# Kernel optimization log

Measured on AMD Instinct MI355X. Metric: run time of the kernel, lower is better.

The kernel has to match this reference:

```python
import jax, jax.numpy as jnp
import numpy as np

B, T, D_IN, UNITS, D_OUT = 64, 2048, 64, 128, 1
ODE_UNFOLDS = 6  # fused semi-implicit Euler sub-steps per timestep


def setup_inputs() -> dict:
    key = jax.random.key(0)
    ks = jax.random.split(key, 8)
    s = lambda fan: 1.0 / np.sqrt(fan).astype(np.float32)
    return {
        "x": jax.random.normal(ks[0], (B, T, D_IN), jnp.float32),
        "kernel": jax.random.normal(ks[1], (D_IN, UNITS), jnp.float32) * s(D_IN),
        "recurrent_kernel": jax.random.normal(ks[2], (UNITS, UNITS), jnp.float32) * s(UNITS),
        "bias": jnp.zeros((UNITS,), jnp.float32),
        "tau": jax.random.uniform(ks[3], (UNITS,), jnp.float32, 0.5, 2.0),  # positive time constants
        "A": jax.random.normal(ks[4], (UNITS,), jnp.float32),  # reversal potentials
        "out_kernel": jax.random.normal(ks[5], (UNITS, D_OUT), jnp.float32) * s(UNITS),
        "out_bias": jnp.zeros((D_OUT,), jnp.float32),
    }


def _ltc_scan(x_proj, recurrent_kernel, tau, A):
    # x_proj: [B, T, U] precomputed input projection (+bias)
    dt = jnp.float32(1.0 / ODE_UNFOLDS)
    inv_tau = 1.0 / tau  # [U]

    def step(h, xp):  # h: [B,U], xp: [B,U]
        # LTC fused ODE solver: semi-implicit Euler, ODE_UNFOLDS sub-steps
        for _ in range(ODE_UNFOLDS):
            f = jax.nn.sigmoid(xp + h @ recurrent_kernel)  # gating nonlinearity
            h = (h + dt * f * A) / (1.0 + dt * (inv_tau + f))
        return h, h

    h0 = jnp.zeros((x_proj.shape[0], tau.shape[0]), x_proj.dtype)
    _, hs = jax.lax.scan(step, h0, jnp.swapaxes(x_proj, 0, 1))  # scan over time
    return jnp.swapaxes(hs, 0, 1)  # [B, T, U]


def reference(x, kernel, recurrent_kernel, bias, tau, A, out_kernel, out_bias):
    # input projection hoisted out of the recurrence (invariant across unfolds)
    x_proj = jnp.einsum("bti,iu->btu", x, kernel) + bias  # [B,T,U]
    hs = _ltc_scan(x_proj, recurrent_kernel, tau, A)       # return_sequences=True
    return hs @ out_kernel + out_bias                       # Dense(output_dim) -> [B,T,1]
```

## Files before the change

kernel.cpp:

```cpp
#include <hip/hip_runtime.h>

#define TSTEPS  2048
#define DIN     64
#define UNITS   128
#define UNFOLDS 6
#define NT      512


template <int CTRL>
__device__ __forceinline__ float dpp_f(float v) {
    return __int_as_float(
        __builtin_amdgcn_mov_dpp(__float_as_int(v), CTRL, 0xF, 0xF, true));
}

typedef _Float16 h16x2 __attribute__((ext_vector_type(2)));

__device__ __forceinline__ float dot2(h16x2 a, h16x2 b, float c) {
#if __has_builtin(__builtin_amdgcn_fdot2)
    return __builtin_amdgcn_fdot2(a, b, c, false);
#else
    return fmaf((float)a.x, (float)b.x, fmaf((float)a.y, (float)b.y, c));
#endif
}

__global__ __launch_bounds__(NT) void ltc_kernel(
    const float* __restrict__ x,
    const float* __restrict__ kern,
    const float* __restrict__ rk,
    const float* __restrict__ bias,
    const float* __restrict__ tau,
    const float* __restrict__ Avec,
    const float* __restrict__ okern,
    const float* __restrict__ obias,
    float* __restrict__ out)
{
    const int b    = blockIdx.x;
    const int tid  = threadIdx.x;
    const int p    = tid & 15;
    const int g    = tid >> 4;
    const int wid  = tid >> 6;
    const int lane = tid & 63;

    __shared__ __align__(16) _Float16 hbuf[2][UNITS];
    __shared__ float part[8];

    h16x2 w2_[4][4];
    #pragma unroll
    for (int m = 0; m < 4; ++m) {
        const float* r0 = rk + (size_t)(8 * p + 2 * m) * UNITS + 4 * g;
        const float* r1 = r0 + UNITS;
        #pragma unroll
        for (int j = 0; j < 4; ++j) {
            h16x2 v; v.x = (_Float16)r0[j]; v.y = (_Float16)r1[j];
            w2_[m][j] = v;
        }
    }
    float kk_[4][4];
    #pragma unroll
    for (int m = 0; m < 4; ++m) {
        float4 v = ((const float4*)(kern + (size_t)(4 * p + m) * UNITS))[g];
        kk_[m][0] = v.x; kk_[m][1] = v.y; kk_[m][2] = v.z; kk_[m][3] = v.w;
    }

    const float dt  = 1.0f / 6.0f;
    const int   sel = ((p & 1) << 1) | ((p >> 1) & 1);
    const int   u_own = 4 * g + sel;
    const float dtA_o  = dt * Avec[u_own];
    const float cden_o = 1.0f + dt / tau[u_own];
    const float cdp_o  = cden_o + dt;
    const float ok_o   = okern[u_own];
    float4 bv = ((const float4*)bias)[g];
    float bias4[4] = {bv.x, bv.y, bv.z, bv.w};
    const float ob = obias[0];

    float h_own = 0.0f;
    if (tid < UNITS) { hbuf[0][tid] = (_Float16)0.f; hbuf[1][tid] = (_Float16)0.f; }

    const float* xb = x + (size_t)b * TSTEPS * DIN;
    float4 xr = *(const float4*)(xb + 4 * p);
    __syncthreads();

    for (int t = 0; t < TSTEPS; ++t) {
        float xp[4];
        #pragma unroll
        for (int i = 0; i < 4; ++i) xp[i] = (p == 0) ? bias4[i] : 0.0f;
        {
            float xrf[4] = {xr.x, xr.y, xr.z, xr.w};
            #pragma unroll
            for (int m = 0; m < 4; ++m)
                #pragma unroll
                for (int i = 0; i < 4; ++i)
                    xp[i] = fmaf(xrf[m], kk_[m][i], xp[i]);
        }
        int tn = (t + 1 < TSTEPS) ? t + 1 : t;
        float4 xn = *(const float4*)(xb + (size_t)tn * DIN + 4 * p);

        #pragma unroll
        for (int s = 0; s < UNFOLDS; ++s) {
            h16x2 hh[4];
            *(uint4*)hh = *(const uint4*)&hbuf[s & 1][8 * p];

            float acc[4] = {xp[0], xp[1], xp[2], xp[3]};
            #pragma unroll
            for (int m = 0; m < 4; ++m)
                #pragma unroll
                for (int j = 0; j < 4; ++j)
                    acc[j] = dot2(hh[m], w2_[m][j], acc[j]);

            const bool b0 = (p & 1) != 0;
            const bool b1 = (p & 2) != 0;
            float a0 = b0 ? acc[2] : acc[0];
            float c0 = b0 ? acc[0] : acc[2];
            float r0 = a0 + dpp_f<0xB1>(c0);
            float a1 = b0 ? acc[3] : acc[1];
            float c1 = b0 ? acc[1] : acc[3];
            float r1 = a1 + dpp_f<0xB1>(c1);
            float a2 = b1 ? r1 : r0;
            float c2 = b1 ? r0 : r1;
            float sv = a2 + dpp_f<0x4E>(c2);
            sv += dpp_f<0x124>(sv);
            sv += dpp_f<0x128>(sv);

            float e   = __expf(-sv);
            float num = fmaf(h_own, e, h_own + dtA_o);
            float den = fmaf(cden_o, e, cdp_o);
            h_own = num * __builtin_amdgcn_rcpf(den);

            if (p < 4) hbuf[(s & 1) ^ 1][u_own] = (_Float16)h_own;

            if (s == UNFOLDS - 1) {
                float q = (p < 4) ? h_own * ok_o : 0.0f;
                q += __shfl_xor(q, 1);
                q += __shfl_xor(q, 2);
                q += __shfl_xor(q, 4);
                q += __shfl_xor(q, 8);
                q += __shfl_xor(q, 16);
                q += __shfl_xor(q, 32);
                if (lane == 0) part[wid] = q;
            }

            asm volatile("s_waitcnt lgkmcnt(0)" ::: "memory");
            __builtin_amdgcn_sched_barrier(0);
            __builtin_amdgcn_s_barrier();
            __builtin_amdgcn_sched_barrier(0);
        }

        if (tid == 0) {
            float r = ob;
            #pragma unroll
            for (int k = 0; k < 8; ++k) r += part[k];
            out[(size_t)b * TSTEPS + t] = r;
        }
        xr = xn;
    }
}

extern "C" void kernel_launch(void* const* d_in, const int* in_sizes, int n_in,
                              void* d_out, int out_size, void* d_ws, size_t ws_size,
                              hipStream_t stream) {
    const float* x     = (const float*)d_in[0];
    const float* kern  = (const float*)d_in[1];
    const float* rk    = (const float*)d_in[2];
    const float* bias  = (const float*)d_in[3];
    const float* tau   = (const float*)d_in[4];
    const float* Avec  = (const float*)d_in[5];
    const float* okern = (const float*)d_in[6];
    const float* obias = (const float*)d_in[7];
    float* out = (float*)d_out;

    ltc_kernel<<<64, NT, 0, stream>>>(
        x, kern, rk, bias, tau, Avec, okern, obias, out);
}
```

Measured before the change: 3.845 ms.

## Shrink block to 128 threads with 4-way K split per unit

Reduces the workgroup from 512 to 128 threads (two waves), giving each thread 32 of the 128 reduction terms for four units instead of 8. The cross-lane reduction drops from five DPP steps to three, and h is written to shared memory as packed fp16 pairs. Fewer waves should make each per-substep barrier cheaper and shorten the serial critical path. In exchange, each thread does more dot-product work and holds far more weights in registers (64 packed recurrent pairs plus 64 input-kernel floats).

```diff
diff --git a/kernel.cpp b/kernel.cpp
--- a/kernel.cpp
+++ b/kernel.cpp
@@ -4,8 +4,10 @@
 #define DIN     64
 #define UNITS   128
 #define UNFOLDS 6
-#define NT      512
-
+#define NT      128
+
+
+typedef _Float16 h16x2 __attribute__((ext_vector_type(2)));
 
 template <int CTRL>
 __device__ __forceinline__ float dpp_f(float v) {
@@ -13,7 +15,11 @@
         __builtin_amdgcn_mov_dpp(__float_as_int(v), CTRL, 0xF, 0xF, true));
 }
 
-typedef _Float16 h16x2 __attribute__((ext_vector_type(2)));
+__device__ __forceinline__ unsigned pack_rne(float a, float b) {
+    unsigned short ua = __builtin_bit_cast(unsigned short, (_Float16)a);
+    unsigned short ub = __builtin_bit_cast(unsigned short, (_Float16)b);
+    return (unsigned)ua | ((unsigned)ub << 16);
+}
 
 __device__ __forceinline__ float dot2(h16x2 a, h16x2 b, float c) {
 #if __has_builtin(__builtin_amdgcn_fdot2)
@@ -36,18 +42,18 @@
 {
     const int b    = blockIdx.x;
     const int tid  = threadIdx.x;
-    const int p    = tid & 15;
-    const int g    = tid >> 4;
-    const int wid  = tid >> 6;
+    const int p    = tid & 3;
+    const int G    = tid >> 2;
+    const int wv   = tid >> 6;
     const int lane = tid & 63;
 
-    __shared__ __align__(16) _Float16 hbuf[2][UNITS];
-    __shared__ float part[8];
-
-    h16x2 w2_[4][4];
-    #pragma unroll
-    for (int m = 0; m < 4; ++m) {
-        const float* r0 = rk + (size_t)(8 * p + 2 * m) * UNITS + 4 * g;
+    __shared__ __align__(16) unsigned hbuf[2][UNITS / 2];
+    __shared__ float part[2];
+
+    h16x2 w2_[16][4];
+    #pragma unroll
+    for (int m = 0; m < 16; ++m) {
+        const float* r0 = rk + (size_t)(32 * p + 2 * m) * UNITS + 4 * G;
         const float* r1 = r0 + UNITS;
         #pragma unroll
         for (int j = 0; j < 4; ++j) {
@@ -55,88 +61,112 @@
             w2_[m][j] = v;
         }
     }
-    float kk_[4][4];
-    #pragma unroll
-    for (int m = 0; m < 4; ++m) {
-        float4 v = ((const float4*)(kern + (size_t)(4 * p + m) * UNITS))[g];
-        kk_[m][0] = v.x; kk_[m][1] = v.y; kk_[m][2] = v.z; kk_[m][3] = v.w;
+    float kk_[16][4];
+    #pragma unroll
+    for (int m = 0; m < 16; ++m) {
+        const float* r0 = kern + (size_t)(16 * p + m) * UNITS + 4 * G;
+        #pragma unroll
+        for (int j = 0; j < 4; ++j) kk_[m][j] = r0[j];
     }
 
-    const float dt  = 1.0f / 6.0f;
-    const int   sel = ((p & 1) << 1) | ((p >> 1) & 1);
-    const int   u_own = 4 * g + sel;
+    const int   u_own = 4 * G + p;
+    const float dt    = 1.0f / 6.0f;
     const float dtA_o  = dt * Avec[u_own];
     const float cden_o = 1.0f + dt / tau[u_own];
     const float cdp_o  = cden_o + dt;
     const float ok_o   = okern[u_own];
-    float4 bv = ((const float4*)bias)[g];
-    float bias4[4] = {bv.x, bv.y, bv.z, bv.w};
+    float bias4[4];
+    #pragma unroll
+    for (int j = 0; j < 4; ++j) bias4[j] = (p == 0) ? bias[4 * G + j] : 0.0f;
     const float ob = obias[0];
 
     float h_own = 0.0f;
-    if (tid < UNITS) { hbuf[0][tid] = (_Float16)0.f; hbuf[1][tid] = (_Float16)0.f; }
+    if (tid < UNITS / 2) { hbuf[0][tid] = 0u; hbuf[1][tid] = 0u; }
 
     const float* xb = x + (size_t)b * TSTEPS * DIN;
-    float4 xr = *(const float4*)(xb + 4 * p);
+    float4 xr[4];
+    #pragma unroll
+    for (int m = 0; m < 4; ++m) xr[m] = *(const float4*)(xb + 16 * p + 4 * m);
     __syncthreads();
 
     for (int t = 0; t < TSTEPS; ++t) {
-        float xp[4];
-        #pragma unroll
-        for (int i = 0; i < 4; ++i) xp[i] = (p == 0) ? bias4[i] : 0.0f;
+        float xp[4] = {bias4[0], bias4[1], bias4[2], bias4[3]};
         {
-            float xrf[4] = {xr.x, xr.y, xr.z, xr.w};
-            #pragma unroll
-            for (int m = 0; m < 4; ++m)
+            float xq[16];
+            #pragma unroll
+            for (int m = 0; m < 4; ++m) {
+                xq[4 * m + 0] = xr[m].x; xq[4 * m + 1] = xr[m].y;
+                xq[4 * m + 2] = xr[m].z; xq[4 * m + 3] = xr[m].w;
+            }
+            #pragma unroll
+            for (int m = 0; m < 16; ++m)
                 #pragma unroll
-                for (int i = 0; i < 4; ++i)
-                    xp[i] = fmaf(xrf[m], kk_[m][i], xp[i]);
+                for (int j = 0; j < 4; ++j)
+                    xp[j] = fmaf(xq[m], kk_[m][j], xp[j]);
         }
+
         int tn = (t + 1 < TSTEPS) ? t + 1 : t;
-        float4 xn = *(const float4*)(xb + (size_t)tn * DIN + 4 * p);
+        float4 xn[4];
+        #pragma unroll
+        for (int m = 0; m < 4; ++m)
+            xn[m] = *(const float4*)(xb + (size_t)tn * DIN + 16 * p + 4 * m);
 
         #pragma unroll
         for (int s = 0; s < UNFOLDS; ++s) {
-            h16x2 hh[4];
-            *(uint4*)hh = *(const uint4*)&hbuf[s & 1][8 * p];
+            h16x2 hh[16];
+            {
+                const uint4* hv = (const uint4*)&hbuf[s & 1][16 * p];
+                *(uint4*)&hh[0]  = hv[0];
+                *(uint4*)&hh[4]  = hv[1];
+                *(uint4*)&hh[8]  = hv[2];
+                *(uint4*)&hh[12] = hv[3];
+            }
 
             float acc[4] = {xp[0], xp[1], xp[2], xp[3]};
-            #pragma unroll
-            for (int m = 0; m < 4; ++m)
+            float accB[4] = {0.f, 0.f, 0.f, 0.f};
+            #pragma unroll
+            for (int m = 0; m < 8; ++m)
                 #pragma unroll
                 for (int j = 0; j < 4; ++j)
                     acc[j] = dot2(hh[m], w2_[m][j], acc[j]);
+            #pragma unroll
+            for (int m = 8; m < 16; ++m)
+                #pragma unroll
+                for (int j = 0; j < 4; ++j)
+                    accB[j] = dot2(hh[m], w2_[m][j], accB[j]);
+            #pragma unroll
+            for (int j = 0; j < 4; ++j) acc[j] += accB[j];
 
             const bool b0 = (p & 1) != 0;
             const bool b1 = (p & 2) != 0;
-            float a0 = b0 ? acc[2] : acc[0];
-            float c0 = b0 ? acc[0] : acc[2];
-            float r0 = a0 + dpp_f<0xB1>(c0);
-            float a1 = b0 ? acc[3] : acc[1];
-            float c1 = b0 ? acc[1] : acc[3];
-            float r1 = a1 + dpp_f<0xB1>(c1);
-            float a2 = b1 ? r1 : r0;
-            float c2 = b1 ? r0 : r1;
-            float sv = a2 + dpp_f<0x4E>(c2);
-            sv += dpp_f<0x124>(sv);
-            sv += dpp_f<0x128>(sv);
+            float k0 = b0 ? acc[1] : acc[0];
+            float s0 = b0 ? acc[0] : acc[1];
+            float k1 = b0 ? acc[3] : acc[2];
+            float s1 = b0 ? acc[2] : acc[3];
+            float r0 = k0 + dpp_f<0xB1>(s0);
+            float r1 = k1 + dpp_f<0xB1>(s1);
+            float k2 = b1 ? r1 : r0;
+            float s2 = b1 ? r0 : r1;
+            float sv = k2 + dpp_f<0x4E>(s2);
 
             float e   = __expf(-sv);
             float num = fmaf(h_own, e, h_own + dtA_o);
             float den = fmaf(cden_o, e, cdp_o);
             h_own = num * __builtin_amdgcn_rcpf(den);
 
-            if (p < 4) hbuf[(s & 1) ^ 1][u_own] = (_Float16)h_own;
+            float hN = dpp_f<0xB1>(h_own);
+            if ((p & 1) == 0)
+                hbuf[(s & 1) ^ 1][2 * G + (p >> 1)] = pack_rne(h_own, hN);
 
             if (s == UNFOLDS - 1) {
-                float q = (p < 4) ? h_own * ok_o : 0.0f;
+                float q = h_own * ok_o;
                 q += __shfl_xor(q, 1);
                 q += __shfl_xor(q, 2);
                 q += __shfl_xor(q, 4);
                 q += __shfl_xor(q, 8);
                 q += __shfl_xor(q, 16);
                 q += __shfl_xor(q, 32);
-                if (lane == 0) part[wid] = q;
+                if (lane == 0) part[wv] = q;
             }
 
             asm volatile("s_waitcnt lgkmcnt(0)" ::: "memory");
@@ -145,13 +175,11 @@
             __builtin_amdgcn_sched_barrier(0);
         }
 
-        if (tid == 0) {
-            float r = ob;
-            #pragma unroll
-            for (int k = 0; k < 8; ++k) r += part[k];
-            out[(size_t)b * TSTEPS + t] = r;
-        }
-        xr = xn;
+        if (tid == 0)
+            out[(size_t)b * TSTEPS + t] = part[0] + part[1] + ob;
+
+        #pragma unroll
+        for (int m = 0; m < 4; ++m) xr[m] = xn[m];
     }
 }
 
```

Result: slower. 4.169 ms (+8.4%).

## Process two batch rows per block to share barriers and weight registers

Applied to the files above, without the earlier changes.

Each block now runs the LTC recurrence for two batch elements at once, keeping both hidden states in separate shared buffers and interleaving their dot-product, reduction and update work between the same barriers. The grid shrinks from 64 to 32 blocks. The intent is to fill the latency-bound per-substep chain with independent work and amortize barrier cost. The trade-off is more work per barrier interval on the serial critical path and fewer concurrent blocks on a GPU that was already underfilled.

```diff
diff --git a/kernel.cpp b/kernel.cpp
--- a/kernel.cpp
+++ b/kernel.cpp
@@ -5,15 +5,16 @@
 #define UNITS   128
 #define UNFOLDS 6
 #define NT      512
-
+#define NB      2
+
+
+typedef _Float16 h16x2 __attribute__((ext_vector_type(2)));
 
 template <int CTRL>
 __device__ __forceinline__ float dpp_f(float v) {
     return __int_as_float(
         __builtin_amdgcn_mov_dpp(__float_as_int(v), CTRL, 0xF, 0xF, true));
 }
-
-typedef _Float16 h16x2 __attribute__((ext_vector_type(2)));
 
 __device__ __forceinline__ float dot2(h16x2 a, h16x2 b, float c) {
 #if __has_builtin(__builtin_amdgcn_fdot2)
@@ -34,15 +35,14 @@
     const float* __restrict__ obias,
     float* __restrict__ out)
 {
-    const int b    = blockIdx.x;
     const int tid  = threadIdx.x;
     const int p    = tid & 15;
     const int g    = tid >> 4;
     const int wid  = tid >> 6;
     const int lane = tid & 63;
 
-    __shared__ __align__(16) _Float16 hbuf[2][UNITS];
-    __shared__ float part[8];
+    __shared__ __align__(16) _Float16 hbuf[2][NB][UNITS];
+    __shared__ float part[NB][8];
 
     h16x2 w2_[4][4];
     #pragma unroll
@@ -73,70 +73,100 @@
     float bias4[4] = {bv.x, bv.y, bv.z, bv.w};
     const float ob = obias[0];
 
-    float h_own = 0.0f;
-    if (tid < UNITS) { hbuf[0][tid] = (_Float16)0.f; hbuf[1][tid] = (_Float16)0.f; }
-
-    const float* xb = x + (size_t)b * TSTEPS * DIN;
-    float4 xr = *(const float4*)(xb + 4 * p);
+    float h_own[NB] = {0.0f, 0.0f};
+    if (tid < UNITS) {
+        hbuf[0][0][tid] = (_Float16)0.f; hbuf[0][1][tid] = (_Float16)0.f;
+        hbuf[1][0][tid] = (_Float16)0.f; hbuf[1][1][tid] = (_Float16)0.f;
+    }
+
+    const float* xb[NB];
+    xb[0] = x + (size_t)(2 * blockIdx.x) * TSTEPS * DIN;
+    xb[1] = xb[0] + (size_t)TSTEPS * DIN;
+    float4 xr[NB];
+    #pragma unroll
+    for (int bt = 0; bt < NB; ++bt) xr[bt] = *(const float4*)(xb[bt] + 4 * p);
     __syncthreads();
 
     for (int t = 0; t < TSTEPS; ++t) {
-        float xp[4];
-        #pragma unroll
-        for (int i = 0; i < 4; ++i) xp[i] = (p == 0) ? bias4[i] : 0.0f;
-        {
-            float xrf[4] = {xr.x, xr.y, xr.z, xr.w};
+        float xp[NB][4];
+        #pragma unroll
+        for (int bt = 0; bt < NB; ++bt) {
+            #pragma unroll
+            for (int i = 0; i < 4; ++i) xp[bt][i] = (p == 0) ? bias4[i] : 0.0f;
+            float xrf[4] = {xr[bt].x, xr[bt].y, xr[bt].z, xr[bt].w};
             #pragma unroll
             for (int m = 0; m < 4; ++m)
                 #pragma unroll
                 for (int i = 0; i < 4; ++i)
-                    xp[i] = fmaf(xrf[m], kk_[m][i], xp[i]);
-        }
+                    xp[bt][i] = fmaf(xrf[m], kk_[m][i], xp[bt][i]);
+        }
+
         int tn = (t + 1 < TSTEPS) ? t + 1 : t;
-        float4 xn = *(const float4*)(xb + (size_t)tn * DIN + 4 * p);
+        float4 xn[NB];
+        #pragma unroll
+        for (int bt = 0; bt < NB; ++bt)
+            xn[bt] = *(const float4*)(xb[bt] + (size_t)tn * DIN + 4 * p);
 
         #pragma unroll
         for (int s = 0; s < UNFOLDS; ++s) {
-            h16x2 hh[4];
-            *(uint4*)hh = *(const uint4*)&hbuf[s & 1][8 * p];
-
-            float acc[4] = {xp[0], xp[1], xp[2], xp[3]};
-            #pragma unroll
-            for (int m = 0; m < 4; ++m)
-                #pragma unroll
-                for (int j = 0; j < 4; ++j)
-                    acc[j] = dot2(hh[m], w2_[m][j], acc[j]);
-
-            const bool b0 = (p & 1) != 0;
-            const bool b1 = (p & 2) != 0;
-            float a0 = b0 ? acc[2] : acc[0];
-            float c0 = b0 ? acc[0] : acc[2];
-            float r0 = a0 + dpp_f<0xB1>(c0);
-            float a1 = b0 ? acc[3] : acc[1];
-            float c1 = b0 ? acc[1] : acc[3];
-            float r1 = a1 + dpp_f<0xB1>(c1);
-            float a2 = b1 ? r1 : r0;
-            float c2 = b1 ? r0 : r1;
-            float sv = a2 + dpp_f<0x4E>(c2);
-            sv += dpp_f<0x124>(sv);
-            sv += dpp_f<0x128>(sv);
-
-            float e   = __expf(-sv);
-            float num = fmaf(h_own, e, h_own + dtA_o);
-            float den = fmaf(cden_o, e, cdp_o);
-            h_own = num * __builtin_amdgcn_rcpf(den);
-
-            if (p < 4) hbuf[(s & 1) ^ 1][u_own] = (_Float16)h_own;
+            const int pp = s & 1;
+
+            h16x2 hh[NB][4];
+            #pragma unroll
+            for (int bt = 0; bt < NB; ++bt)
+                *(uint4*)&hh[bt][0] = *(const uint4*)&hbuf[pp][bt][8 * p];
+
+            float sv[NB];
+            #pragma unroll
+            for (int bt = 0; bt < NB; ++bt) {
+                float acc[4] = {xp[bt][0], xp[bt][1], xp[bt][2], xp[bt][3]};
+                #pragma unroll
+                for (int m = 0; m < 4; ++m)
+                    #pragma unroll
+                    for (int j = 0; j < 4; ++j)
+                        acc[j] = dot2(hh[bt][m], w2_[m][j], acc[j]);
+
+                const bool b0 = (p & 1) != 0;
+                const bool b1 = (p & 2) != 0;
+                float a0 = b0 ? acc[2] : acc[0];
+                float c0 = b0 ? acc[0] : acc[2];
+                float r0 = a0 + dpp_f<0xB1>(c0);
+                float a1 = b0 ? acc[3] : acc[1];
+                float c1 = b0 ? acc[1] : acc[3];
+                float r1 = a1 + dpp_f<0xB1>(c1);
+                float a2 = b1 ? r1 : r0;
+                float c2 = b1 ? r0 : r1;
+                float v  = a2 + dpp_f<0x4E>(c2);
+                v += dpp_f<0x124>(v);
+                v += dpp_f<0x128>(v);
+                sv[bt] = v;
+            }
+
+            #pragma unroll
+            for (int bt = 0; bt < NB; ++bt) {
+                float e   = __expf(-sv[bt]);
+                float num = fmaf(h_own[bt], e, h_own[bt] + dtA_o);
+                float den = fmaf(cden_o, e, cdp_o);
+                h_own[bt] = num * __builtin_amdgcn_rcpf(den);
+            }
+
+            if (p < 4) {
+                hbuf[pp ^ 1][0][u_own] = (_Float16)h_own[0];
+                hbuf[pp ^ 1][1][u_own] = (_Float16)h_own[1];
+            }
 
             if (s == UNFOLDS - 1) {
-                float q = (p < 4) ? h_own * ok_o : 0.0f;
-                q += __shfl_xor(q, 1);
-                q += __shfl_xor(q, 2);
-                q += __shfl_xor(q, 4);
-                q += __shfl_xor(q, 8);
-                q += __shfl_xor(q, 16);
-                q += __shfl_xor(q, 32);
-                if (lane == 0) part[wid] = q;
+                #pragma unroll
+                for (int bt = 0; bt < NB; ++bt) {
+                    float q = (p < 4) ? h_own[bt] * ok_o : 0.0f;
+                    q += __shfl_xor(q, 1);
+                    q += __shfl_xor(q, 2);
+                    q += __shfl_xor(q, 4);
+                    q += __shfl_xor(q, 8);
+                    q += __shfl_xor(q, 16);
+                    q += __shfl_xor(q, 32);
+                    if (lane == 0) part[bt][wid] = q;
+                }
             }
 
             asm volatile("s_waitcnt lgkmcnt(0)" ::: "memory");
@@ -146,12 +176,16 @@
         }
 
         if (tid == 0) {
-            float r = ob;
-            #pragma unroll
-            for (int k = 0; k < 8; ++k) r += part[k];
-            out[(size_t)b * TSTEPS + t] = r;
-        }
-        xr = xn;
+            #pragma unroll
+            for (int bt = 0; bt < NB; ++bt) {
+                float r = ob;
+                #pragma unroll
+                for (int k = 0; k < 8; ++k) r += part[bt][k];
+                out[(size_t)(2 * blockIdx.x + bt) * TSTEPS + t] = r;
+            }
+        }
+        #pragma unroll
+        for (int bt = 0; bt < NB; ++bt) xr[bt] = xn[bt];
     }
 }
 
@@ -168,6 +202,6 @@
     const float* obias = (const float*)d_in[7];
     float* out = (float*)d_out;
 
-    ltc_kernel<<<64, NT, 0, stream>>>(
+    ltc_kernel<<<64 / NB, NT, 0, stream>>>(
         x, kern, rk, bias, tau, Avec, okern, obias, out);
 }
```

Measured after the change: 5.717 ms. +48.7%, slower.
